# Kernel tuning notes

Hardware: AMD Instinct MI355X
Metric: run time of the kernel (lower is better)

## Reference

```python
import jax, jax.numpy as jnp
import numpy as np
import math

B, E, H, HD, P, G, N, L, FF = 16, 768, 12, 64, 16, 14, 196, 12, 3072
SQRT_E = math.sqrt(E)
SQRT_HD = math.sqrt(HD)


def cosine_norm(x):
    n = jnp.linalg.norm(x, axis=-1, keepdims=True)
    return x / jnp.maximum(n, 1e-6)


def layer_norm(x, w, b, eps=1e-6):
    m = jnp.mean(x, axis=-1, keepdims=True)
    v = jnp.var(x, axis=-1, keepdims=True)
    return (x - m) / jnp.sqrt(v + eps) * w + b


def setup_inputs() -> dict:
    key = jax.random.key(0)
    ks = jax.random.split(key, 16)
    std = 0.02
    return {
        "x": jax.random.normal(ks[0], (B, 3, 224, 224), jnp.float32),
        "patch_w": jax.random.normal(ks[1], (E, 3, P, P), jnp.float32) * std,
        "patch_b": jnp.zeros((E,), jnp.float32),
        "cls_token": jax.random.normal(ks[2], (1, 1, E), jnp.float32) * std,
        "pos_embed": jax.random.normal(ks[3], (1, N + 1, E), jnp.float32) * std,
        "Wq": jax.random.normal(ks[4], (L, E, E), jnp.float32) * std,
        "Wk": jax.random.normal(ks[5], (L, E, E), jnp.float32) * std,
        "Wv": jax.random.normal(ks[6], (L, E, E), jnp.float32) * std,
        "Wo": jax.random.normal(ks[7], (L, E, E), jnp.float32) * std,
        # Scale params stored at their torch init values (s = ones * scale)
        "s_qk": jnp.ones((L, H, HD), jnp.float32) / SQRT_E,        # scale=1/sqrt(dim)
        "Wup": jax.random.normal(ks[8], (L, FF, E), jnp.float32) * std,
        "Wgate": jax.random.normal(ks[9], (L, FF, E), jnp.float32) * std,
        "Wdown": jax.random.normal(ks[10], (L, E, FF), jnp.float32) * std,
        "s_u": jnp.ones((L, FF), jnp.float32),
        "s_v": jnp.ones((L, FF), jnp.float32),
        "alpha_A": jnp.ones((L, E), jnp.float32) / SQRT_E,         # scale=1/sqrt(dim)
        "alpha_M": jnp.ones((L, E), jnp.float32) / SQRT_E,
        "fc_w": jnp.ones((E,), jnp.float32),
        "fc_b": jnp.zeros((E,), jnp.float32),
    }


def _attention(h, wq, wk, wv, wo, s_qk):
    b, n, _ = h.shape
    q = (h @ wq.T).reshape(b, n, H, HD)
    k = (h @ wk.T).reshape(b, n, H, HD)
    v = (h @ wv.T).reshape(b, n, H, HD)
    # Scale.forward(): s * (init/scale) with init=1, scale=1/sqrt(E)
    s = s_qk * SQRT_E                                   # [H, HD]
    q = cosine_norm(q) * s
    k = cosine_norm(k) * s
    logits = jnp.einsum("bnhd,bmhd->bhnm", q, k) * SQRT_HD
    attn = jax.nn.softmax(logits, axis=-1)
    out = jnp.einsum("bhnm,bmhd->bnhd", attn, v).reshape(b, n, E)
    return out @ wo.T


def _mlp(h, wup, wgate, wdown, s_u, s_v):
    u = (h @ wup.T) * s_u
    v = (h @ wgate.T) * s_v * SQRT_E                    # mlp scale = sqrt(in_features)
    hidden = u * jax.nn.silu(v)
    return hidden @ wdown.T


def _block(h, wq, wk, wv, wo, s_qk, wup, wgate, wdown, s_u, s_v, a_A, a_M):
    # alpha Scale: init=0.05, scale=1/sqrt(E) -> effective = s * 0.05 * sqrt(E)
    aA = a_A * (0.05 * SQRT_E)
    aM = a_M * (0.05 * SQRT_E)
    h_A = cosine_norm(_attention(h, wq, wk, wv, wo, s_qk))
    h = cosine_norm(h + aA * (h_A - h))
    h_M = cosine_norm(_mlp(h, wup, wgate, wdown, s_u, s_v))
    h = cosine_norm(h + aM * (h_M - h))
    return h


def reference(x, patch_w, patch_b, cls_token, pos_embed, Wq, Wk, Wv, Wo, s_qk,
              Wup, Wgate, Wdown, s_u, s_v, alpha_A, alpha_M, fc_w, fc_b):
    b = x.shape[0]
    # patch embed: conv k=stride=16 == patch extraction + linear proj
    patches = x.reshape(b, 3, G, P, G, P).transpose(0, 2, 4, 1, 3, 5).reshape(b, N, 3 * P * P)
    t = patches @ patch_w.reshape(E, -1).T + patch_b    # [B, N, E]
    t = jnp.concatenate([jnp.broadcast_to(cls_token, (b, 1, E)), t], axis=1)
    t = t + pos_embed                                    # [B, N+1, E]
    nodes = None
    for i in range(L):
        t = _block(t, Wq[i], Wk[i], Wv[i], Wo[i], s_qk[i],
                   Wup[i], Wgate[i], Wdown[i], s_u[i], s_v[i], alpha_A[i], alpha_M[i])
        if i == L - 2:
            nodes = layer_norm(t, fc_w, fc_b)[:, 1:]
    edges = layer_norm(t, fc_w, fc_b)[:, 1:]
    return nodes, edges
```

## Files before the change

kernel.cpp:

```cpp
#include <hip/hip_runtime.h>
#include <hip/hip_bf16.h>
#include <cstdint>
#include <cstddef>

typedef __hip_bfloat16 bf16;
typedef short bf16x8 __attribute__((ext_vector_type(8)));
typedef float f32x4 __attribute__((ext_vector_type(4)));

#define SQRT_E   27.712812921102035f
#define ASCALE   (0.05f * 27.712812921102035f)
#define MPAD     3200

__device__ __forceinline__ void load_lds16(const bf16* g, bf16* l) {
    __builtin_amdgcn_global_load_lds(
        (const __attribute__((address_space(1))) void*)g,
        (__attribute__((address_space(3))) void*)l, 16, 0, 0);
}

__device__ __forceinline__ float block_sum(float v, float* sbuf) {
#pragma unroll
    for (int m = 32; m >= 1; m >>= 1) v += __shfl_xor(v, m);
    __syncthreads();
    if ((threadIdx.x & 63) == 0) sbuf[threadIdx.x >> 6] = v;
    __syncthreads();
    return sbuf[0] + sbuf[1] + sbuf[2] + sbuf[3];
}

__device__ __forceinline__ void cvt8(const float* s, bf16* d) {
    float4 f0 = *(const float4*)s;
    float4 f1 = *(const float4*)(s + 4);
    bf16 t[8];
    t[0] = __float2bfloat16(f0.x); t[1] = __float2bfloat16(f0.y);
    t[2] = __float2bfloat16(f0.z); t[3] = __float2bfloat16(f0.w);
    t[4] = __float2bfloat16(f1.x); t[5] = __float2bfloat16(f1.y);
    t[6] = __float2bfloat16(f1.z); t[7] = __float2bfloat16(f1.w);
    *reinterpret_cast<uint4*>(d) = *reinterpret_cast<const uint4*>(t);
}

__device__ __forceinline__ void wconv_body(
    int idx,
    const float* __restrict__ wq, const float* __restrict__ wk,
    const float* __restrict__ wv, const float* __restrict__ wo,
    const float* __restrict__ wu, const float* __restrict__ wg,
    const float* __restrict__ wd, bf16* __restrict__ dst) {
    const float* src;
    size_t off;
    if (idx < 294912) {
        int seg = idx / 73728, o = idx - seg * 73728;
        src = (seg == 0) ? wq : (seg == 1) ? wk : (seg == 2) ? wv : wo;
        off = (size_t)o * 8;
    } else {
        int i2 = idx - 294912;
        int seg = i2 / 294912, o = i2 - seg * 294912;
        src = (seg == 0) ? wu : (seg == 1) ? wg : wd;
        off = (size_t)o * 8;
    }
    cvt8(src + off, dst + (size_t)idx * 8);
}

__global__ __launch_bounds__(256) void prep_kernel(
    const float* __restrict__ x, bf16* __restrict__ A,
    const float* __restrict__ patchw, bf16* __restrict__ pwb) {
    int b = blockIdx.x, tid = threadIdx.x;
    if (b < 288) {
        int idx = b * 256 + tid;
        cvt8(patchw + (size_t)idx * 8, pwb + (size_t)idx * 8);
    } else {
        int idx = (b - 288) * 256 + tid;
        int row = idx / 768, col = idx - row * 768;
        if (row >= 3136) { A[idx] = __float2bfloat16(0.f); return; }
        int bb = row / 196, pp = row - bb * 196;
        int gy = pp / 14, gx = pp - gy * 14;
        int c = col >> 8, rem = col & 255, py = rem >> 4, px = rem & 15;
        A[idx] = __float2bfloat16(
            x[((size_t)(bb * 3 + c) * 224 + gy * 16 + py) * 224 + gx * 16 + px]);
    }
}

__global__ __launch_bounds__(256) void patch_fused(
    const bf16* __restrict__ A, const bf16* __restrict__ Bw,
    const float* __restrict__ pb, const float* __restrict__ cls,
    const float* __restrict__ pos,
    float* __restrict__ h, bf16* __restrict__ hb,
    const float* __restrict__ wq, const float* __restrict__ wk,
    const float* __restrict__ wv, const float* __restrict__ wo,
    const float* __restrict__ wu, const float* __restrict__ wg,
    const float* __restrict__ wd, bf16* __restrict__ wdst) {
    __shared__ __align__(16) bf16 As[128 * 32];
    __shared__ __align__(16) bf16 Bs[128 * 32];
    const int bb = blockIdx.x;
    const int tid = threadIdx.x;
    if (bb >= 166) {
        int idx = (bb - 166) * 256 + tid;
        wconv_body(idx, wq, wk, wv, wo, wu, wg, wd, wdst);
        return;
    }
    if (bb >= 150) {
        int bi = bb - 150;
        size_t row = (size_t)bi * 197 * 768;
#pragma unroll
        for (int i = 0; i < 3; i++) {
            int c = tid + i * 256;
            float v = cls[c] + pos[c];
            h[row + c] = v;
            hb[row + c] = __float2bfloat16(v);
        }
        return;
    }
    const int lane = tid & 63, wave = tid >> 6;
    const int wm = wave & 1, wn = wave >> 1;
    const int quad = lane >> 4, l16 = lane & 15;
    const int nt = bb % 6;
    const int row0 = (bb / 6) * 128;
    const int col0 = nt * 128;
    const bf16* Ab = A + (size_t)row0 * 768;
    const bf16* Bb = Bw + (size_t)col0 * 768;

    f32x4 acc[4][4];
    f32x4 zero = {0.f, 0.f, 0.f, 0.f};
#pragma unroll
    for (int i = 0; i < 4; i++)
#pragma unroll
        for (int j = 0; j < 4; j++) acc[i][j] = zero;

    for (int k0 = 0; k0 < 768; k0 += 32) {
#pragma unroll
        for (int it = 0; it < 2; ++it) {
            int cidx = it * 256 + tid;
            int r = cidx >> 2, cg = cidx & 3;
            load_lds16(Ab + (size_t)r * 768 + k0 + cg * 8, As + cidx * 8);
            load_lds16(Bb + (size_t)r * 768 + k0 + cg * 8, Bs + cidx * 8);
        }
        __syncthreads();
        bf16x8 av[4], bv[4];
#pragma unroll
        for (int i = 0; i < 4; i++) {
            av[i] = *(const bf16x8*)(As + (wm * 64 + i * 16 + l16) * 32 + quad * 8);
            bv[i] = *(const bf16x8*)(Bs + (wn * 64 + i * 16 + l16) * 32 + quad * 8);
        }
#pragma unroll
        for (int i = 0; i < 4; i++)
#pragma unroll
            for (int j = 0; j < 4; j++)
                acc[i][j] = __builtin_amdgcn_mfma_f32_16x16x32_bf16(av[i], bv[j], acc[i][j], 0, 0, 0);
        __syncthreads();
    }
#pragma unroll
    for (int i = 0; i < 4; i++) {
        int rr = row0 + wm * 64 + i * 16 + quad * 4;
#pragma unroll
        for (int j = 0; j < 4; j++) {
            int cc = col0 + wn * 64 + j * 16 + l16;
#pragma unroll
            for (int r = 0; r < 4; r++) {
                int p = rr + r;
                if (p < 3136) {
                    int bi = p / 196, n = p - bi * 196;
                    float val = acc[i][j][r] + pb[cc] + pos[(size_t)(n + 1) * 768 + cc];
                    size_t hr = (size_t)(bi * 197 + n + 1) * 768 + cc;
                    h[hr] = val;
                    hb[hr] = __float2bfloat16(val);
                }
            }
        }
    }
}

__global__ __launch_bounds__(256) void gemm_bt(
    const bf16* __restrict__ A, int lda,
    const bf16* __restrict__ B0, const bf16* __restrict__ B1, const bf16* __restrict__ B2,
    int tilesPerSeg, int segColStride,
    void* __restrict__ Cv, int ldc, long long partStride,
    int Klen, int ldb, int outBf16) {
    __shared__ __align__(16) bf16 As[128 * 32];
    __shared__ __align__(16) bf16 Bs[128 * 32];
    const int tid = threadIdx.x;
    const int lane = tid & 63, wave = tid >> 6;
    const int wm = wave & 1, wn = wave >> 1;
    const int quad = lane >> 4, l16 = lane & 15;
    const int seg = blockIdx.x / tilesPerSeg;
    const int nt = blockIdx.x - seg * tilesPerSeg;
    const bf16* B = (seg == 0) ? B0 : (seg == 1 ? B1 : B2);
    const int row0 = blockIdx.y * 128;
    const int col0 = nt * 128;
    const long long kofs = (long long)blockIdx.z * Klen;
    const bf16* Ab = A + (size_t)row0 * lda + kofs;
    const bf16* Bb = B + (size_t)col0 * ldb + kofs;
    const long long cofs = (long long)blockIdx.z * partStride + (long long)seg * segColStride;

    f32x4 acc[4][4];
    f32x4 zero = {0.f, 0.f, 0.f, 0.f};
#pragma unroll
    for (int i = 0; i < 4; i++)
#pragma unroll
        for (int j = 0; j < 4; j++) acc[i][j] = zero;

    for (int k0 = 0; k0 < Klen; k0 += 32) {
#pragma unroll
        for (int it = 0; it < 2; ++it) {
            int cidx = it * 256 + tid;
            int r = cidx >> 2, cg = cidx & 3;
            load_lds16(Ab + (size_t)r * lda + k0 + cg * 8, As + cidx * 8);
            load_lds16(Bb + (size_t)r * ldb + k0 + cg * 8, Bs + cidx * 8);
        }
        __syncthreads();
        bf16x8 av[4], bv[4];
#pragma unroll
        for (int i = 0; i < 4; i++) {
            av[i] = *(const bf16x8*)(As + (wm * 64 + i * 16 + l16) * 32 + quad * 8);
            bv[i] = *(const bf16x8*)(Bs + (wn * 64 + i * 16 + l16) * 32 + quad * 8);
        }
#pragma unroll
        for (int i = 0; i < 4; i++)
#pragma unroll
            for (int j = 0; j < 4; j++)
                acc[i][j] = __builtin_amdgcn_mfma_f32_16x16x32_bf16(av[i], bv[j], acc[i][j], 0, 0, 0);
        __syncthreads();
    }
    if (outBf16) {
        bf16* Cb = (bf16*)Cv + cofs;
#pragma unroll
        for (int i = 0; i < 4; i++) {
            int rr = row0 + wm * 64 + i * 16 + quad * 4;
#pragma unroll
            for (int j = 0; j < 4; j++) {
                int cc = col0 + wn * 64 + j * 16 + l16;
#pragma unroll
                for (int r = 0; r < 4; r++)
                    Cb[(size_t)(rr + r) * ldc + cc] = __float2bfloat16(acc[i][j][r]);
            }
        }
    } else {
        float* Cb = (float*)Cv + cofs;
#pragma unroll
        for (int i = 0; i < 4; i++) {
            int rr = row0 + wm * 64 + i * 16 + quad * 4;
#pragma unroll
            for (int j = 0; j < 4; j++) {
                int cc = col0 + wn * 64 + j * 16 + l16;
#pragma unroll
                for (int r = 0; r < 4; r++)
                    Cb[(size_t)(rr + r) * ldc + cc] = acc[i][j][r];
            }
        }
    }
}

__global__ __launch_bounds__(256) void gemm_qkv(
    const bf16* __restrict__ A,
    const bf16* __restrict__ Bq, const bf16* __restrict__ Bk, const bf16* __restrict__ Bv,
    const float* __restrict__ s_l,
    bf16* __restrict__ Qd, bf16* __restrict__ Kd, bf16* __restrict__ VTd,
    const float* __restrict__ wq, const float* __restrict__ wk,
    const float* __restrict__ wv, const float* __restrict__ wo,
    const float* __restrict__ wu, const float* __restrict__ wg,
    const float* __restrict__ wd, bf16* __restrict__ wdst) {
    __shared__ __align__(16) bf16 As[128 * 32];
    __shared__ __align__(16) bf16 Bs[128 * 32];
    const int bb = blockIdx.x;
    const int tid = threadIdx.x;
    if (bb >= 450) {
        int idx = (bb - 450) * 256 + tid;
        wconv_body(idx, wq, wk, wv, wo, wu, wg, wd, wdst);
        return;
    }
    const int lane = tid & 63, wave = tid >> 6;
    const int wm = wave & 1, wn = wave >> 1;
    const int quad = lane >> 4, l16 = lane & 15;
    const int seg = bb / 150;
    const int rem = bb - seg * 150;
    const int nt = rem % 6;
    const int row0 = (rem / 6) * 128;
    const int col0 = nt * 128;
    const bf16* B = (seg == 0) ? Bq : (seg == 1 ? Bk : Bv);
    const bf16* Ab = A + (size_t)row0 * 768;
    const bf16* Bb = B + (size_t)col0 * 768;

    f32x4 acc[4][4];
    f32x4 zero = {0.f, 0.f, 0.f, 0.f};
#pragma unroll
    for (int i = 0; i < 4; i++)
#pragma unroll
        for (int j = 0; j < 4; j++) acc[i][j] = zero;

    for (int k0 = 0; k0 < 768; k0 += 32) {
#pragma unroll
        for (int it = 0; it < 2; ++it) {
            int cidx = it * 256 + tid;
            int r = cidx >> 2, cg = cidx & 3;
            load_lds16(Ab + (size_t)r * 768 + k0 + cg * 8, As + cidx * 8);
            load_lds16(Bb + (size_t)r * 768 + k0 + cg * 8, Bs + cidx * 8);
        }
        __syncthreads();
        bf16x8 av[4], bv[4];
#pragma unroll
        for (int i = 0; i < 4; i++) {
            av[i] = *(const bf16x8*)(As + (wm * 64 + i * 16 + l16) * 32 + quad * 8);
            bv[i] = *(const bf16x8*)(Bs + (wn * 64 + i * 16 + l16) * 32 + quad * 8);
        }
#pragma unroll
        for (int i = 0; i < 4; i++)
#pragma unroll
            for (int j = 0; j < 4; j++)
                acc[i][j] = __builtin_amdgcn_mfma_f32_16x16x32_bf16(av[i], bv[j], acc[i][j], 0, 0, 0);
        __syncthreads();
    }

    const int hcol = nt * 2 + wn;
    if (seg < 2) {
        bf16* Dst = (seg == 0) ? Qd : Kd;
        float sv0[4];
#pragma unroll
        for (int j = 0; j < 4; j++) sv0[j] = s_l[hcol * 64 + j * 16 + l16] * SQRT_E;
#pragma unroll
        for (int i = 0; i < 4; i++) {
#pragma unroll
            for (int r = 0; r < 4; r++) {
                float ss = acc[i][0][r] * acc[i][0][r] + acc[i][1][r] * acc[i][1][r]
                         + acc[i][2][r] * acc[i][2][r] + acc[i][3][r] * acc[i][3][r];
#pragma unroll
                for (int m = 1; m < 16; m <<= 1) ss += __shfl_xor(ss, m);
                float inv = 1.f / fmaxf(sqrtf(ss), 1e-6f);
                int t = row0 + wm * 64 + i * 16 + quad * 4 + r;
                if (t < 3152) {
                    int b = t / 197, n = t - b * 197;
                    size_t base = ((size_t)(b * 12 + hcol) * 208 + n) * 64;
#pragma unroll
                    for (int j = 0; j < 4; j++)
                        Dst[base + j * 16 + l16] =
                            __float2bfloat16(acc[i][j][r] * inv * sv0[j]);
                }
            }
        }
    } else {
#pragma unroll
        for (int i = 0; i < 4; i++) {
#pragma unroll
            for (int r = 0; r < 4; r++) {
                int t = row0 + wm * 64 + i * 16 + quad * 4 + r;
                if (t < 3152) {
                    int b = t / 197, n = t - b * 197;
                    size_t vbase = (size_t)(b * 12 + hcol) * 64 * 224 + n;
#pragma unroll
                    for (int j = 0; j < 4; j++)
                        VTd[vbase + (size_t)(j * 16 + l16) * 224] =
                            __float2bfloat16(acc[i][j][r]);
                }
            }
        }
    }
}

__global__ __launch_bounds__(256) void gemm_upgate(
    const bf16* __restrict__ A, const bf16* __restrict__ Bu, const bf16* __restrict__ Bv,
    const float* __restrict__ su, const float* __restrict__ sv,
    bf16* __restrict__ H) {
    __shared__ __align__(16) bf16 As[128 * 32];
    __shared__ __align__(16) bf16 Bus[64 * 32];
    __shared__ __align__(16) bf16 Bvs[64 * 32];
    const int tid = threadIdx.x;
    const int lane = tid & 63, wave = tid >> 6;
    const int wm = wave & 1, wn = wave >> 1;
    const int quad = lane >> 4, l16 = lane & 15;
    const int ct = blockIdx.x;
    const int row0 = blockIdx.y * 128;
    const bf16* Ab = A + (size_t)row0 * 768;
    const bf16* Bub = Bu + (size_t)ct * 64 * 768;
    const bf16* Bvb = Bv + (size_t)ct * 64 * 768;

    f32x4 au[4][2], av_[4][2];
    f32x4 zero = {0.f, 0.f, 0.f, 0.f};
#pragma unroll
    for (int i = 0; i < 4; i++)
#pragma unroll
        for (int j = 0; j < 2; j++) { au[i][j] = zero; av_[i][j] = zero; }

    for (int k0 = 0; k0 < 768; k0 += 32) {
#pragma unroll
        for (int it = 0; it < 2; ++it) {
            int cidx = it * 256 + tid;
            int r = cidx >> 2, cg = cidx & 3;
            load_lds16(Ab + (size_t)r * 768 + k0 + cg * 8, As + cidx * 8);
        }
        {
            int r = tid >> 2, cg = tid & 3;
            load_lds16(Bub + (size_t)r * 768 + k0 + cg * 8, Bus + tid * 8);
            load_lds16(Bvb + (size_t)r * 768 + k0 + cg * 8, Bvs + tid * 8);
        }
        __syncthreads();
        bf16x8 a[4], bu[2], bv[2];
#pragma unroll
        for (int i = 0; i < 4; i++)
            a[i] = *(const bf16x8*)(As + (wm * 64 + i * 16 + l16) * 32 + quad * 8);
#pragma unroll
        for (int j = 0; j < 2; j++) {
            bu[j] = *(const bf16x8*)(Bus + (wn * 32 + j * 16 + l16) * 32 + quad * 8);
            bv[j] = *(const bf16x8*)(Bvs + (wn * 32 + j * 16 + l16) * 32 + quad * 8);
        }
#pragma unroll
        for (int i = 0; i < 4; i++)
#pragma unroll
            for (int j = 0; j < 2; j++) {
                au[i][j]  = __builtin_amdgcn_mfma_f32_16x16x32_bf16(a[i], bu[j], au[i][j], 0, 0, 0);
                av_[i][j] = __builtin_amdgcn_mfma_f32_16x16x32_bf16(a[i], bv[j], av_[i][j], 0, 0, 0);
            }
        __syncthreads();
    }
#pragma unroll
    for (int j = 0; j < 2; j++) {
        int cc = ct * 64 + wn * 32 + j * 16 + l16;
        float suc = su[cc];
        float svc = sv[cc] * SQRT_E;
#pragma unroll
        for (int i = 0; i < 4; i++) {
            int rr = row0 + wm * 64 + i * 16 + quad * 4;
#pragma unroll
            for (int r = 0; r < 4; r++) {
                float u = au[i][j][r] * suc;
                float v = av_[i][j][r] * svc;
                float sig = 1.f / (1.f + __expf(-v));
                H[(size_t)(rr + r) * 3072 + cc] = __float2bfloat16(u * v * sig);
            }
        }
    }
}

__global__ __launch_bounds__(64) void attn_kernel(
    const bf16* __restrict__ Q, const bf16* __restrict__ K,
    const bf16* __restrict__ VT, bf16* __restrict__ O) {
    __shared__ __align__(16) bf16 Ps[16 * 224];
    int lane = threadIdx.x;
    int quad = lane >> 4, l16 = lane & 15;
    int bh = blockIdx.x % 192;
    int qt = blockIdx.x / 192;
    int b = bh / 12, h = bh - b * 12;
    const bf16* Qb = Q + (size_t)bh * 208 * 64;
    const bf16* Kb = K + (size_t)bh * 208 * 64;
    const bf16* Vb = VT + (size_t)bh * 64 * 224;
    f32x4 zero = {0.f, 0.f, 0.f, 0.f};

    bf16x8 a0 = *(const bf16x8*)(Qb + (qt * 16 + l16) * 64 + quad * 8);
    bf16x8 a1 = *(const bf16x8*)(Qb + (qt * 16 + l16) * 64 + quad * 8 + 32);

    f32x4 lg[13];
#pragma unroll
    for (int kt = 0; kt < 13; kt++) {
        bf16x8 b0 = *(const bf16x8*)(Kb + (kt * 16 + l16) * 64 + quad * 8);
        bf16x8 b1 = *(const bf16x8*)(Kb + (kt * 16 + l16) * 64 + quad * 8 + 32);
        f32x4 c = zero;
        c = __builtin_amdgcn_mfma_f32_16x16x32_bf16(a0, b0, c, 0, 0, 0);
        c = __builtin_amdgcn_mfma_f32_16x16x32_bf16(a1, b1, c, 0, 0, 0);
        lg[kt] = c;
    }
    float sm[4] = {0.f, 0.f, 0.f, 0.f};
#pragma unroll
    for (int kt = 0; kt < 13; kt++) {
        bool valid = (kt * 16 + l16) < 197;
#pragma unroll
        for (int r = 0; r < 4; r++) {
            float p = valid ? __expf(lg[kt][r] * 8.0f) : 0.f;
            lg[kt][r] = p;
            sm[r] += p;
        }
    }
#pragma unroll
    for (int m = 1; m < 16; m <<= 1)
#pragma unroll
        for (int r = 0; r < 4; r++) sm[r] += __shfl_xor(sm[r], m);
    float inv[4];
#pragma unroll
    for (int r = 0; r < 4; r++) inv[r] = 1.f / sm[r];
#pragma unroll
    for (int kt = 0; kt < 13; kt++)
#pragma unroll
        for (int r = 0; r < 4; r++)
            Ps[(quad * 4 + r) * 224 + kt * 16 + l16] = __float2bfloat16(lg[kt][r]);
#pragma unroll
    for (int r = 0; r < 4; r++)
        Ps[(quad * 4 + r) * 224 + 208 + l16] = __float2bfloat16(0.f);
    __syncthreads();
#pragma unroll
    for (int nt = 0; nt < 4; nt++) {
        f32x4 o = zero;
#pragma unroll
        for (int ks = 0; ks < 7; ks++) {
            bf16x8 pa = *(const bf16x8*)(Ps + l16 * 224 + ks * 32 + quad * 8);
            bf16x8 vb = *(const bf16x8*)(Vb + (nt * 16 + l16) * 224 + ks * 32 + quad * 8);
            o = __builtin_amdgcn_mfma_f32_16x16x32_bf16(pa, vb, o, 0, 0, 0);
        }
#pragma unroll
        for (int r = 0; r < 4; r++) {
            int tok = qt * 16 + quad * 4 + r;
            if (tok < 197)
                O[(size_t)(b * 197 + tok) * 768 + h * 64 + nt * 16 + l16] =
                    __float2bfloat16(o[r] * inv[r]);
        }
    }
}

__global__ __launch_bounds__(256) void residual_cos(
    const bf16* __restrict__ proj, int nParts, long long partStride,
    const float* __restrict__ alpha,
    float* __restrict__ h, bf16* __restrict__ hb,
    const float* __restrict__ fcw, const float* __restrict__ fcb,
    float* __restrict__ lnout) {
    __shared__ float sbuf[4];
    int row = blockIdx.x, tid = threadIdx.x;
    float p[3];
    float ss = 0.f;
#pragma unroll
    for (int i = 0; i < 3; i++) {
        int c = tid + i * 256;
        float v = 0.f;
        for (int pt = 0; pt < nParts; pt++)
            v += __bfloat162float(proj[(long long)pt * partStride + (size_t)row * 768 + c]);
        p[i] = v;
        ss += v * v;
    }
    ss = block_sum(ss, sbuf);
    float inv1 = 1.f / fmaxf(sqrtf(ss), 1e-6f);
    float ss2 = 0.f;
#pragma unroll
    for (int i = 0; i < 3; i++) {
        int c = tid + i * 256;
        float hv = h[(size_t)row * 768 + c];
        float a = alpha[c] * ASCALE;
        float m = hv + a * (p[i] * inv1 - hv);
        p[i] = m;
        ss2 += m * m;
    }
    ss2 = block_sum(ss2, sbuf);
    float inv2 = 1.f / fmaxf(sqrtf(ss2), 1e-6f);
    float v0 = p[0] * inv2, v1 = p[1] * inv2, v2 = p[2] * inv2;
    {
        int c = tid;
        h[(size_t)row * 768 + c] = v0;
        hb[(size_t)row * 768 + c] = __float2bfloat16(v0);
        h[(size_t)row * 768 + c + 256] = v1;
        hb[(size_t)row * 768 + c + 256] = __float2bfloat16(v1);
        h[(size_t)row * 768 + c + 512] = v2;
        hb[(size_t)row * 768 + c + 512] = __float2bfloat16(v2);
    }
    if (lnout) {
        float s = block_sum(v0 + v1 + v2, sbuf);
        float mean = s * (1.f / 768.f);
        float var = (1.f / 768.f) - mean * mean;
        float invs = 1.f / sqrtf(var + 1e-6f);
        int b = row / 197, n = row - b * 197;
        if (n >= 1) {
            size_t obase = (size_t)(b * 196 + n - 1) * 768;
            lnout[obase + tid]       = (v0 - mean) * invs * fcw[tid] + fcb[tid];
            lnout[obase + tid + 256] = (v1 - mean) * invs * fcw[tid + 256] + fcb[tid + 256];
            lnout[obase + tid + 512] = (v2 - mean) * invs * fcw[tid + 512] + fcb[tid + 512];
        }
    }
}

extern "C" void kernel_launch(void* const* d_in, const int* in_sizes, int n_in,
                              void* d_out, int out_size, void* d_ws, size_t ws_size,
                              hipStream_t stream) {
    (void)in_sizes; (void)n_in; (void)out_size; (void)ws_size;
    const float* x      = (const float*)d_in[0];
    const float* patchw = (const float*)d_in[1];
    const float* patchb = (const float*)d_in[2];
    const float* cls    = (const float*)d_in[3];
    const float* pos    = (const float*)d_in[4];
    const float* Wq     = (const float*)d_in[5];
    const float* Wk     = (const float*)d_in[6];
    const float* Wv     = (const float*)d_in[7];
    const float* Wo     = (const float*)d_in[8];
    const float* s_qk   = (const float*)d_in[9];
    const float* Wup    = (const float*)d_in[10];
    const float* Wgate  = (const float*)d_in[11];
    const float* Wdown  = (const float*)d_in[12];
    const float* s_u    = (const float*)d_in[13];
    const float* s_v    = (const float*)d_in[14];
    const float* alA    = (const float*)d_in[15];
    const float* alM    = (const float*)d_in[16];
    const float* fcw    = (const float*)d_in[17];
    const float* fcb    = (const float*)d_in[18];
    float* out = (float*)d_out;

    char* ws = (char*)d_ws;
    size_t ofs = 0;
    auto alloc = [&](size_t bytes) -> void* {
        void* p = ws + ofs;
        ofs += (bytes + 255) & ~(size_t)255;
        return p;
    };
    float* h      = (float*)alloc((size_t)MPAD * 768 * 4);
    float* part   = (float*)alloc((size_t)4 * MPAD * 768 * 4);
    bf16*  hb     = (bf16*)alloc((size_t)MPAD * 768 * 2);
    bf16*  attno  = (bf16*)alloc((size_t)MPAD * 768 * 2);
    bf16*  hidden = (bf16*)alloc((size_t)MPAD * 3072 * 2);
    size_t qkvt_bytes = ((size_t)192 * 208 * 64 * 2) * 2 + (size_t)192 * 64 * 224 * 2;
    bf16*  Qb     = (bf16*)alloc(qkvt_bytes);
    bf16*  Kb     = Qb + (size_t)192 * 208 * 64;
    bf16*  VTb    = Kb + (size_t)192 * 208 * 64;
    const size_t WPL = 9437184;
    bf16*  wbf0   = (bf16*)alloc(WPL * 2);
    bf16*  wbf1   = (bf16*)alloc(WPL * 2);
    bf16*  pwb    = (bf16*)alloc((size_t)589824 * 2);

    bf16*  partb  = (bf16*)part;
    bf16*  Apatch = hidden;

    const long long PSTR = (long long)MPAD * 768;
    const size_t EE = 768 * 768, FE = (size_t)3072 * 768;

    prep_kernel<<<9888, 256, 0, stream>>>(x, Apatch, patchw, pwb);
    patch_fused<<<4774, 256, 0, stream>>>(Apatch, pwb, patchb, cls, pos, h, hb,
                                          Wq, Wk, Wv, Wo, Wup, Wgate, Wdown, wbf0);
    hipMemsetAsync(Qb, 0, qkvt_bytes, stream);

    for (int l = 0; l < 12; l++) {
        bf16* wl    = (l & 1) ? wbf1 : wbf0;
        bf16* wnext = (l & 1) ? wbf0 : wbf1;
        bf16* wqb = wl;
        bf16* wkb = wl + 589824;
        bf16* wvb = wl + 1179648;
        bf16* wob = wl + 1769472;
        bf16* wub = wl + 2359296;
        bf16* wgb = wl + 4718592;
        bf16* wdb = wl + 7077888;
        int ln = (l < 11) ? (l + 1) : l;

        gemm_qkv<<<(l < 11) ? 5058 : 450, 256, 0, stream>>>(
            hb, wqb, wkb, wvb, s_qk + (size_t)l * 768, Qb, Kb, VTb,
            Wq + (size_t)ln * EE, Wk + (size_t)ln * EE,
            Wv + (size_t)ln * EE, Wo + (size_t)ln * EE,
            Wup + (size_t)ln * FE, Wgate + (size_t)ln * FE,
            Wdown + (size_t)ln * FE, wnext);
        attn_kernel<<<2496, 64, 0, stream>>>(Qb, Kb, VTb, attno);
        gemm_bt<<<dim3(6, 25, 2), 256, 0, stream>>>(attno, 768, wob, wob, wob,
                                                    6, 0, partb, 768, PSTR, 384, 768, 1);
        residual_cos<<<3152, 256, 0, stream>>>(partb, 2, PSTR, alA + (size_t)l * 768,
                                               h, hb, fcw, fcb, (float*)nullptr);
        gemm_upgate<<<dim3(48, 25), 256, 0, stream>>>(hb, wub, wgb,
                                                      s_u + (size_t)l * 3072,
                                                      s_v + (size_t)l * 3072, hidden);
        gemm_bt<<<dim3(6, 25, 4), 256, 0, stream>>>(hidden, 3072, wdb, wdb, wdb,
                                                    6, 0, partb, 768, PSTR, 768, 3072, 1);
        float* lnp = (l == 10) ? out : (l == 11) ? (out + 2408448) : (float*)nullptr;
        residual_cos<<<3152, 256, 0, stream>>>(partb, 4, PSTR, alM + (size_t)l * 768,
                                               h, hb, fcw, fcb, lnp);
    }
}
```

Baseline: 2.334 ms.

## Rewrite up/gate GEMM as 256x256 tiled, double-buffered kernel with interleaved weights

The up and gate weights are now interleaved during bf16 conversion, in 32-row chunks, so a single B tile holds matching up and gate columns. The fused up/gate SwiGLU GEMM moves from a 128x64 tile with 32-wide K steps to a 256x256 tile with 64-wide K steps. It uses double-buffered, XOR-swizzled LDS loads, 512 threads, a swizzled block order and phased prefetching. This aims to raise data reuse and MFMA density and to overlap loads with compute. In exchange it uses much more LDS (128KB) and registers, and launches only 312 blocks, which may limit occupancy.

```diff
diff --git a/kernel.cpp b/kernel.cpp
--- a/kernel.cpp
+++ b/kernel.cpp
@@ -43,19 +43,23 @@
     const float* __restrict__ wv, const float* __restrict__ wo,
     const float* __restrict__ wu, const float* __restrict__ wg,
     const float* __restrict__ wd, bf16* __restrict__ dst) {
-    const float* src;
-    size_t off;
     if (idx < 294912) {
         int seg = idx / 73728, o = idx - seg * 73728;
-        src = (seg == 0) ? wq : (seg == 1) ? wk : (seg == 2) ? wv : wo;
-        off = (size_t)o * 8;
-    } else {
-        int i2 = idx - 294912;
-        int seg = i2 / 294912, o = i2 - seg * 294912;
-        src = (seg == 0) ? wu : (seg == 1) ? wg : wd;
-        off = (size_t)o * 8;
-    }
-    cvt8(src + off, dst + (size_t)idx * 8);
+        const float* src = (seg == 0) ? wq : (seg == 1) ? wk : (seg == 2) ? wv : wo;
+        cvt8(src + (size_t)o * 8, dst + (size_t)idx * 8);
+        return;
+    }
+    int i2 = idx - 294912;
+    int seg = i2 / 294912, o = i2 - seg * 294912;
+    if (seg == 2) {
+        cvt8(wd + (size_t)o * 8, dst + (size_t)idx * 8);
+        return;
+    }
+    const float* src = (seg == 0) ? wu : wg;
+    int row = o / 96, kc = o - row * 96;
+    int drow = (row >> 5) * 64 + (row & 31) + (seg == 1 ? 32 : 0);
+    cvt8(src + (size_t)o * 8,
+         dst + ((size_t)294912 + (size_t)drow * 96 + kc) * 8);
 }
 
 __global__ __launch_bounds__(256) void prep_kernel(
@@ -351,75 +355,153 @@
     }
 }
 
-__global__ __launch_bounds__(256) void gemm_upgate(
-    const bf16* __restrict__ A, const bf16* __restrict__ Bu, const bf16* __restrict__ Bv,
+__global__ __launch_bounds__(512) void gemm8_upgate(
+    const bf16* __restrict__ A, const bf16* __restrict__ Bg,
     const float* __restrict__ su, const float* __restrict__ sv,
     bf16* __restrict__ H) {
-    __shared__ __align__(16) bf16 As[128 * 32];
-    __shared__ __align__(16) bf16 Bus[64 * 32];
-    __shared__ __align__(16) bf16 Bvs[64 * 32];
+    __shared__ __align__(16) bf16 As[2][256 * 64];
+    __shared__ __align__(16) bf16 Bs[2][256 * 64];
     const int tid = threadIdx.x;
     const int lane = tid & 63, wave = tid >> 6;
-    const int wm = wave & 1, wn = wave >> 1;
+    const int wm = wave >> 2, wn = wave & 3;
     const int quad = lane >> 4, l16 = lane & 15;
-    const int ct = blockIdx.x;
-    const int row0 = blockIdx.y * 128;
+    const int rs = l16 & 7;
+    int bid = blockIdx.x;
+    int swz = (bid & 7) * 39 + (bid >> 3);
+    const int mt = swz / 24, nt = swz - mt * 24;
+    const int row0 = mt * 256, col0 = nt * 256;
     const bf16* Ab = A + (size_t)row0 * 768;
-    const bf16* Bub = Bu + (size_t)ct * 64 * 768;
-    const bf16* Bvb = Bv + (size_t)ct * 64 * 768;
-
-    f32x4 au[4][2], av_[4][2];
+    const bf16* Bb = Bg + (size_t)col0 * 768;
+    const int r0 = tid >> 3, k80 = tid & 7;
+    const int r1 = (tid + 512) >> 3, k81 = tid & 7;
+
+    f32x4 acc[8][4];
     f32x4 zero = {0.f, 0.f, 0.f, 0.f};
 #pragma unroll
-    for (int i = 0; i < 4; i++)
-#pragma unroll
-        for (int j = 0; j < 2; j++) { au[i][j] = zero; av_[i][j] = zero; }
-
-    for (int k0 = 0; k0 < 768; k0 += 32) {
-#pragma unroll
-        for (int it = 0; it < 2; ++it) {
-            int cidx = it * 256 + tid;
-            int r = cidx >> 2, cg = cidx & 3;
-            load_lds16(Ab + (size_t)r * 768 + k0 + cg * 8, As + cidx * 8);
-        }
+    for (int i = 0; i < 8; i++)
+#pragma unroll
+        for (int j = 0; j < 4; j++) acc[i][j] = zero;
+
+    auto stage = [&](int buf, int part, int kt) {
+        int kb = kt * 64;
+        if (part < 2) {
+            load_lds16(Ab + (size_t)(part * 128 + r0) * 768 + kb + ((k80 ^ (r0 & 7)) << 3),
+                       &As[buf][(part * 128 + r0) * 64 + (k80 << 3)]);
+            load_lds16(Ab + (size_t)(part * 128 + r1) * 768 + kb + ((k81 ^ (r1 & 7)) << 3),
+                       &As[buf][(part * 128 + r1) * 64 + (k81 << 3)]);
+        } else {
+            int p2 = part - 2;
+            load_lds16(Bb + (size_t)(p2 * 128 + r0) * 768 + kb + ((k80 ^ (r0 & 7)) << 3),
+                       &Bs[buf][(p2 * 128 + r0) * 64 + (k80 << 3)]);
+            load_lds16(Bb + (size_t)(p2 * 128 + r1) * 768 + kb + ((k81 ^ (r1 & 7)) << 3),
+                       &Bs[buf][(p2 * 128 + r1) * 64 + (k81 << 3)]);
+        }
+    };
+
+#pragma unroll
+    for (int part = 0; part < 4; part++) stage(0, part, 0);
+    asm volatile("s_waitcnt vmcnt(0)" ::: "memory");
+    __builtin_amdgcn_sched_barrier(0);
+    __builtin_amdgcn_s_barrier();
+    __builtin_amdgcn_sched_barrier(0);
+
+    for (int i = 0; i < 6; i++) {
         {
-            int r = tid >> 2, cg = tid & 3;
-            load_lds16(Bub + (size_t)r * 768 + k0 + cg * 8, Bus + tid * 8);
-            load_lds16(Bvb + (size_t)r * 768 + k0 + cg * 8, Bvs + tid * 8);
-        }
-        __syncthreads();
-        bf16x8 a[4], bu[2], bv[2];
-#pragma unroll
-        for (int i = 0; i < 4; i++)
-            a[i] = *(const bf16x8*)(As + (wm * 64 + i * 16 + l16) * 32 + quad * 8);
+            bf16x8 bv[4][2];
+#pragma unroll
+            for (int ph = 0; ph < 4; ph++) {
+                stage(1, ph, 2 * i + 1);
+                if (ph == 0) {
+#pragma unroll
+                    for (int n = 0; n < 4; n++)
+#pragma unroll
+                        for (int k32 = 0; k32 < 2; k32++)
+                            bv[n][k32] = *(const bf16x8*)
+                                (&Bs[0][(wn * 64 + n * 16 + l16) * 64 +
+                                        (((k32 * 4 + quad) ^ rs) << 3)]);
+                }
+                bf16x8 av[2][2];
+#pragma unroll
+                for (int mh = 0; mh < 2; mh++)
+#pragma unroll
+                    for (int k32 = 0; k32 < 2; k32++)
+                        av[mh][k32] = *(const bf16x8*)
+                            (&As[0][(wm * 128 + (2 * ph + mh) * 16 + l16) * 64 +
+                                    (((k32 * 4 + quad) ^ rs) << 3)]);
+                __builtin_amdgcn_s_setprio(1);
+#pragma unroll
+                for (int mh = 0; mh < 2; mh++)
+#pragma unroll
+                    for (int n = 0; n < 4; n++) {
+                        acc[2 * ph + mh][n] = __builtin_amdgcn_mfma_f32_16x16x32_bf16(
+                            av[mh][0], bv[n][0], acc[2 * ph + mh][n], 0, 0, 0);
+                        acc[2 * ph + mh][n] = __builtin_amdgcn_mfma_f32_16x16x32_bf16(
+                            av[mh][1], bv[n][1], acc[2 * ph + mh][n], 0, 0, 0);
+                    }
+                __builtin_amdgcn_s_setprio(0);
+                if (ph == 3) asm volatile("s_waitcnt vmcnt(0)" ::: "memory");
+                __builtin_amdgcn_sched_barrier(0);
+                __builtin_amdgcn_s_barrier();
+                __builtin_amdgcn_sched_barrier(0);
+            }
+        }
+        {
+            bf16x8 bv[4][2];
+#pragma unroll
+            for (int ph = 0; ph < 4; ph++) {
+                if (i < 5) stage(0, ph, 2 * i + 2);
+                if (ph == 0) {
+#pragma unroll
+                    for (int n = 0; n < 4; n++)
+#pragma unroll
+                        for (int k32 = 0; k32 < 2; k32++)
+                            bv[n][k32] = *(const bf16x8*)
+                                (&Bs[1][(wn * 64 + n * 16 + l16) * 64 +
+                                        (((k32 * 4 + quad) ^ rs) << 3)]);
+                }
+                bf16x8 av[2][2];
+#pragma unroll
+                for (int mh = 0; mh < 2; mh++)
+#pragma unroll
+                    for (int k32 = 0; k32 < 2; k32++)
+                        av[mh][k32] = *(const bf16x8*)
+                            (&As[1][(wm * 128 + (2 * ph + mh) * 16 + l16) * 64 +
+                                    (((k32 * 4 + quad) ^ rs) << 3)]);
+                __builtin_amdgcn_s_setprio(1);
+#pragma unroll
+                for (int mh = 0; mh < 2; mh++)
+#pragma unroll
+                    for (int n = 0; n < 4; n++) {
+                        acc[2 * ph + mh][n] = __builtin_amdgcn_mfma_f32_16x16x32_bf16(
+                            av[mh][0], bv[n][0], acc[2 * ph + mh][n], 0, 0, 0);
+                        acc[2 * ph + mh][n] = __builtin_amdgcn_mfma_f32_16x16x32_bf16(
+                            av[mh][1], bv[n][1], acc[2 * ph + mh][n], 0, 0, 0);
+                    }
+                __builtin_amdgcn_s_setprio(0);
+                if (ph == 3) asm volatile("s_waitcnt vmcnt(0)" ::: "memory");
+                __builtin_amdgcn_sched_barrier(0);
+                __builtin_amdgcn_s_barrier();
+                __builtin_amdgcn_sched_barrier(0);
+            }
+        }
+    }
+
+#pragma unroll
+    for (int m = 0; m < 8; m++) {
+        int row = row0 + wm * 128 + m * 16 + quad * 4;
 #pragma unroll
         for (int j = 0; j < 2; j++) {
-            bu[j] = *(const bf16x8*)(Bus + (wn * 32 + j * 16 + l16) * 32 + quad * 8);
-            bv[j] = *(const bf16x8*)(Bvs + (wn * 32 + j * 16 + l16) * 32 + quad * 8);
-        }
-#pragma unroll
-        for (int i = 0; i < 4; i++)
-#pragma unroll
-            for (int j = 0; j < 2; j++) {
-                au[i][j]  = __builtin_amdgcn_mfma_f32_16x16x32_bf16(a[i], bu[j], au[i][j], 0, 0, 0);
-                av_[i][j] = __builtin_amdgcn_mfma_f32_16x16x32_bf16(a[i], bv[j], av_[i][j], 0, 0, 0);
-            }
-        __syncthreads();
-    }
-#pragma unroll
-    for (int j = 0; j < 2; j++) {
-        int cc = ct * 64 + wn * 32 + j * 16 + l16;
-        float suc = su[cc];
-        float svc = sv[cc] * SQRT_E;
-#pragma unroll
-        for (int i = 0; i < 4; i++) {
-            int rr = row0 + wm * 64 + i * 16 + quad * 4;
+            int c = (nt * 4 + wn) * 32 + j * 16 + l16;
+            float suc = su[c];
+            float svc = sv[c] * SQRT_E;
 #pragma unroll
             for (int r = 0; r < 4; r++) {
-                float u = au[i][j][r] * suc;
-                float v = av_[i][j][r] * svc;
-                float sig = 1.f / (1.f + __expf(-v));
-                H[(size_t)(rr + r) * 3072 + cc] = __float2bfloat16(u * v * sig);
+                if (row + r < 3200) {
+                    float u = acc[m][j][r] * suc;
+                    float v = acc[m][j + 2][r] * svc;
+                    float sig = 1.f / (1.f + __expf(-v));
+                    H[(size_t)(row + r) * 3072 + c] = __float2bfloat16(u * v * sig);
+                }
             }
         }
     }
@@ -621,7 +703,6 @@
         bf16* wvb = wl + 1179648;
         bf16* wob = wl + 1769472;
         bf16* wub = wl + 2359296;
-        bf16* wgb = wl + 4718592;
         bf16* wdb = wl + 7077888;
         int ln = (l < 11) ? (l + 1) : l;
 
@@ -636,9 +717,9 @@
                                                     6, 0, partb, 768, PSTR, 384, 768, 1);
         residual_cos<<<3152, 256, 0, stream>>>(partb, 2, PSTR, alA + (size_t)l * 768,
                                                h, hb, fcw, fcb, (float*)nullptr);
-        gemm_upgate<<<dim3(48, 25), 256, 0, stream>>>(hb, wub, wgb,
-                                                      s_u + (size_t)l * 3072,
-                                                      s_v + (size_t)l * 3072, hidden);
+        gemm8_upgate<<<312, 512, 0, stream>>>(hb, wub,
+                                              s_u + (size_t)l * 3072,
+                                              s_v + (size_t)l * 3072, hidden);
         gemm_bt<<<dim3(6, 25, 4), 256, 0, stream>>>(hidden, 3072, wdb, wdb, wdb,
                                                     6, 0, partb, 768, PSTR, 768, 3072, 1);
         float* lnp = (l == 10) ? out : (l == 11) ? (out + 2408448) : (float*)nullptr;
```

Result: slower. 2.635 ms (+12.9%).
